# Kernel optimization log

Measured on AMD Instinct MI355X. Metric: run time of the kernel, lower is better.

## Reference

```python
import jax, jax.numpy as jnp
import numpy as np

N = 100000       # num_nodes
E = 1200000      # num_edges
D = 64           # input feature dim
K = 10           # propagation iterations
ALPHA = 0.1      # teleport probability
H0, H1 = 64, 32  # units_list


def setup_inputs() -> dict:
    key = jax.random.key(0)
    ks = jax.random.split(key, 5)
    x = jax.random.normal(ks[0], (N, D), dtype=jnp.float32)
    edge_index = jax.random.randint(ks[1], (2, E), 0, N, dtype=jnp.int32)
    edge_weight = jax.random.uniform(ks[2], (E,), dtype=jnp.float32)
    # glorot-ish dense params per units_list=[64, 32]
    W0 = jax.random.normal(ks[3], (D, H0), dtype=jnp.float32) * (1.0 / np.sqrt(D))
    b0 = jnp.zeros((H0,), jnp.float32)
    W1 = jax.random.normal(ks[4], (H0, H1), dtype=jnp.float32) * (1.0 / np.sqrt(H0))
    b1 = jnp.zeros((H1,), jnp.float32)
    return dict(x=x, edge_index=edge_index, edge_weight=edge_weight,
                W0=W0, b0=b0, W1=W1, b1=b1)


def reference(x, edge_index, edge_weight, W0, b0, W1, b1):
    n = x.shape[0]
    loop = jnp.arange(n, dtype=edge_index.dtype)
    # GCN renorm: add self-loops with fill weight 1, symmetric D^-1/2 A D^-1/2
    row = jnp.concatenate([edge_index[0], loop])
    col = jnp.concatenate([edge_index[1], loop])
    w = jnp.concatenate([edge_weight, jnp.ones((n,), x.dtype)])
    deg = jax.ops.segment_sum(w, row, num_segments=n)
    dinv = jax.lax.rsqrt(jnp.maximum(deg, 1e-12))
    nw = dinv[row] * w * dinv[col]          # [E+N] normalized edge weights

    # k-hop propagation with running sum: (1/K) sum_k A_hat^k x
    h = x
    acc = jnp.zeros_like(x)
    for _ in range(K):
        h = jax.ops.segment_sum(nw[:, None] * h[row], col, num_segments=n)
        acc = acc + h
    out = acc * ((1.0 - ALPHA) / K) + ALPHA * x

    # dense MLP stack: all but last activated with relu, last linear
    out = jax.nn.relu(out @ W0 + b0)
    out = out @ W1 + b1
    return out
```

## Files before the change

kernel.cpp:

```cpp
#include <hip/hip_runtime.h>
#include <hip/hip_bf16.h>

#define NTHREADS 256
#define GB 256
#define NB 256
#define BW 512

typedef unsigned int uint32;
typedef unsigned long long u64;
typedef __bf16 bf16x8 __attribute__((ext_vector_type(8)));
typedef float f32x4 __attribute__((ext_vector_type(4)));


__device__ __forceinline__ float blo(uint32 u) { return __uint_as_float(u << 16); }
__device__ __forceinline__ float bhi(uint32 u) { return __uint_as_float(u & 0xffff0000u); }

__device__ __forceinline__ unsigned short bf16bits(float f) {
    __hip_bfloat16 h = __float2bfloat16(f);
    return *reinterpret_cast<unsigned short*>(&h);
}
__device__ __forceinline__ uint32 pk2(float a, float b) {
    return (uint32)bf16bits(a) | ((uint32)bf16bits(b) << 16);
}


__global__ __launch_bounds__(256) void histcols_k(const int* __restrict__ row,
                                                  const int* __restrict__ col,
                                                  int* __restrict__ bh, int* __restrict__ bh2,
                                                  int e, int ch) {
    __shared__ int h1[NB], h2[NB];
    int tid = threadIdx.x;
    h1[tid] = 0; h2[tid] = 0;
    __syncthreads();
    int beg = blockIdx.x * ch;
    int end = min(e, beg + ch);
    for (int i = beg + tid; i < end; i += 256) {
        atomicAdd(&h1[col[i] >> 9], 1);
        atomicAdd(&h2[row[i] >> 9], 1);
    }
    __syncthreads();
    bh[(size_t)tid * GB + blockIdx.x] = h1[tid];
    bh2[(size_t)tid * GB + blockIdx.x] = h2[tid];
}


__global__ __launch_bounds__(256) void scanb_k(int* bh, int* tb) {
    __shared__ int s[GB];
    int b = blockIdx.x;
    int tid = threadIdx.x;
    size_t base = (size_t)b * GB + tid;
    int v = bh[base];
    s[tid] = v;
    __syncthreads();
    for (int off = 1; off < GB; off <<= 1) {
        int t = (tid >= off) ? s[tid - off] : 0;
        __syncthreads();
        s[tid] += t;
        __syncthreads();
    }
    bh[base] = s[tid] - v;
    if (tid == GB - 1) tb[b] = s[GB - 1];
}


__global__ void scant_k(const int* __restrict__ tb, int* gbase) {
    __shared__ int s[256];
    int tid = threadIdx.x;
    int v = tb[tid];
    s[tid] = v;
    __syncthreads();
    for (int off = 1; off < 256; off <<= 1) {
        int t = (tid >= off) ? s[tid - off] : 0;
        __syncthreads();
        s[tid] += t;
        __syncthreads();
    }
    gbase[tid] = s[tid] - v;
    if (tid == 255) gbase[256] = s[255];
}


__global__ __launch_bounds__(256) void bscatter_k(const int* __restrict__ row,
                                                  const int* __restrict__ col,
                                                  const float* __restrict__ w,
                                                  const int* __restrict__ bh,
                                                  const int* __restrict__ bh2,
                                                  const int* __restrict__ gb,
                                                  const int* __restrict__ gb2,
                                                  unsigned short* __restrict__ st_col,
                                                  u64* __restrict__ st_rw,
                                                  u64* __restrict__ st2,
                                                  int e, int ch) {
    __shared__ int h1[NB], h2[NB];
    int tid = threadIdx.x;
    h1[tid] = 0; h2[tid] = 0;
    __syncthreads();
    int beg = blockIdx.x * ch;
    int end = min(e, beg + ch);
    for (int i = beg + tid; i < end; i += 256) {
        int c = col[i], r = row[i];
        float wv = w[i];
        u64 rec = (u64)(uint32)r | ((u64)__float_as_uint(wv) << 32);
        int bk = c >> 9;
        int rank = atomicAdd(&h1[bk], 1);
        int slot = gb[bk] + bh[(size_t)bk * GB + blockIdx.x] + rank;
        st_col[slot] = (unsigned short)(c & (BW - 1));
        st_rw[slot] = rec;
        int bk2 = r >> 9;
        int rank2 = atomicAdd(&h2[bk2], 1);
        int slot2 = gb2[bk2] + bh2[(size_t)bk2 * GB + blockIdx.x] + rank2;
        st2[slot2] = rec;
    }
}


__global__ __launch_bounds__(256) void bdeg_k(const u64* __restrict__ st2,
                                              const int* __restrict__ gb2,
                                              float* __restrict__ dinv, int n) {
    __shared__ float facc[BW];
    int bk = blockIdx.x;
    int tid = threadIdx.x;
    facc[tid] = 0.f; facc[tid + 256] = 0.f;
    __syncthreads();
    int beg = gb2[bk], end = gb2[bk + 1];
    for (int j = beg + tid; j < end; j += 256) {
        u64 v = st2[j];
        int r = (int)(uint32)v;
        float wv = __uint_as_float((uint32)(v >> 32));
        atomicAdd(&facc[r & (BW - 1)], wv);
    }
    __syncthreads();
    int n0 = bk * BW + tid, n1 = n0 + 256;
    if (n0 < n) dinv[n0] = rsqrtf(fmaxf(facc[tid] + 1.f, 1e-12f));
    if (n1 < n) dinv[n1] = rsqrtf(fmaxf(facc[tid + 256] + 1.f, 1e-12f));
}


__global__ __launch_bounds__(256) void bcount_k(const unsigned short* __restrict__ st_col,
                                                const int* __restrict__ gb,
                                                int* __restrict__ counts, int n) {
    __shared__ int cnt[BW];
    int bk = blockIdx.x;
    int tid = threadIdx.x;
    cnt[tid] = 0; cnt[tid + 256] = 0;
    __syncthreads();
    int beg = gb[bk], end = gb[bk + 1];
    for (int j = beg + tid; j < end; j += 256)
        atomicAdd(&cnt[st_col[j]], 1);
    __syncthreads();
    int n0 = bk * BW + tid, n1 = n0 + 256;
    if (n0 < n) counts[n0] = cnt[tid];
    if (n1 < n) counts[n1] = cnt[tid + 256];
}


__global__ void scan1_k(const int* __restrict__ counts, int* offsets, int* blockSums, int n) {
    __shared__ int s[256];
    int tid = threadIdx.x;
    int idx = blockIdx.x * 256 + tid;
    int v = (idx < n) ? counts[idx] : 0;
    s[tid] = v;
    __syncthreads();
    for (int off = 1; off < 256; off <<= 1) {
        int t = (tid >= off) ? s[tid - off] : 0;
        __syncthreads();
        s[tid] += t;
        __syncthreads();
    }
    if (idx < n) offsets[idx] = s[tid] - v;
    if (tid == 255) blockSums[blockIdx.x] = s[255];
}

__global__ void scan2_k(int* blockSums, int nb) {
    __shared__ int s[1024];
    int tid = threadIdx.x;
    int v = (tid < nb) ? blockSums[tid] : 0;
    s[tid] = v;
    __syncthreads();
    for (int off = 1; off < 1024; off <<= 1) {
        int t = (tid >= off) ? s[tid - off] : 0;
        __syncthreads();
        s[tid] += t;
        __syncthreads();
    }
    if (tid < nb) blockSums[tid] = s[tid] - v;
}

__global__ void scan3_k(int* offsets, const int* __restrict__ blockSums, int n, int total) {
    int idx = blockIdx.x * blockDim.x + threadIdx.x;
    if (idx < n) offsets[idx] += blockSums[idx >> 8];
    if (idx == n) offsets[n] = total;
}


__global__ __launch_bounds__(256) void bplace_k(const unsigned short* __restrict__ st_col,
                                                const u64* __restrict__ st_rw,
                                                const int* __restrict__ gb,
                                                const int* __restrict__ offsets,
                                                u64* __restrict__ csr) {
    __shared__ int cnt[BW];
    int bk = blockIdx.x;
    int tid = threadIdx.x;
    cnt[tid] = 0; cnt[tid + 256] = 0;
    __syncthreads();
    int beg = gb[bk], end = gb[bk + 1];
    for (int j = beg + tid; j < end; j += 256) {
        int c9 = st_col[j];
        int rank = atomicAdd(&cnt[c9], 1);
        int node = (bk << 9) | c9;
        csr[offsets[node] + rank] = st_rw[j];
    }
}


__global__ void uxseed_k(const float* __restrict__ x, const float* __restrict__ dinv,
                         uint32* __restrict__ ux, int pairs) {
    int i = blockIdx.x * blockDim.x + threadIdx.x;
    if (i < pairs) {
        float di = dinv[i >> 5];
        float2 v = ((const float2*)x)[i];
        ux[i] = pk2(di * v.x, di * v.y);
    }
}


template <int MODE>
__global__ __launch_bounds__(256) void horner4n_k(
    const unsigned short* __restrict__ u_in,
    unsigned short* __restrict__ u_out,
    unsigned short* __restrict__ ybf,
    const unsigned short* __restrict__ ux_bf,
    const float* __restrict__ x,
    const float* __restrict__ dinv,
    const int* __restrict__ offsets,
    const u64* __restrict__ csr,
    int n)
{
    int wv = __builtin_amdgcn_readfirstlane(threadIdx.x >> 6);
    int lane = threadIdx.x & 63;
    int g = lane >> 3;
    int s = lane & 7;
    int nbase = blockIdx.x * 16 + wv * 4;

    int bb[4], ee[4];
#pragma unroll
    for (int m = 0; m < 4; ++m) {
        int node = nbase + m;
        if (node < n) { bb[m] = offsets[node]; ee[m] = offsets[node + 1]; }
        else          { bb[m] = 0; ee[m] = 0; }
    }
    int maxd = max(max(ee[0] - bb[0], ee[1] - bb[1]), max(ee[2] - bb[2], ee[3] - bb[3]));

    float acc[4][8];
#pragma unroll
    for (int m = 0; m < 4; ++m)
#pragma unroll
        for (int i = 0; i < 8; ++i) acc[m][i] = 0.f;

    u64 sw[4];
#pragma unroll
    for (int m = 0; m < 4; ++m) {
        int j = bb[m] + g;
        sw[m] = (j < ee[m]) ? csr[j] : 0ull;
    }

    for (int off = 0; off < maxd; off += 8) {
        uint4 q[4];
#pragma unroll
        for (int m = 0; m < 4; ++m)
            q[m] = ((const uint4*)(u_in + (size_t)(uint32)(sw[m] & 0xffffffffu) * 64))[s];
        u64 swn[4];
#pragma unroll
        for (int m = 0; m < 4; ++m) {
            int j = bb[m] + off + 8 + g;
            swn[m] = (j < ee[m]) ? csr[j] : 0ull;
        }
#pragma unroll
        for (int m = 0; m < 4; ++m) {
            float w = __uint_as_float((uint32)(sw[m] >> 32));
            acc[m][0] = fmaf(w, blo(q[m].x), acc[m][0]);
            acc[m][1] = fmaf(w, bhi(q[m].x), acc[m][1]);
            acc[m][2] = fmaf(w, blo(q[m].y), acc[m][2]);
            acc[m][3] = fmaf(w, bhi(q[m].y), acc[m][3]);
            acc[m][4] = fmaf(w, blo(q[m].z), acc[m][4]);
            acc[m][5] = fmaf(w, bhi(q[m].z), acc[m][5]);
            acc[m][6] = fmaf(w, blo(q[m].w), acc[m][6]);
            acc[m][7] = fmaf(w, bhi(q[m].w), acc[m][7]);
        }
#pragma unroll
        for (int m = 0; m < 4; ++m) sw[m] = swn[m];
    }

#pragma unroll
    for (int mask = 8; mask <= 32; mask <<= 1)
#pragma unroll
        for (int m = 0; m < 4; ++m)
#pragma unroll
            for (int i = 0; i < 8; ++i)
                acc[m][i] += __shfl_xor(acc[m][i], mask);

    float t[8];
#pragma unroll
    for (int i = 0; i < 8; ++i) {
        float a01 = (g == 0) ? acc[0][i] : acc[1][i];
        float a23 = (g == 2) ? acc[2][i] : acc[3][i];
        t[i] = (g < 2) ? a01 : a23;
    }

    if (g < 4) {
        int node = nbase + g;
        if (node < n) {
            float di = dinv[node];
            uint4 zq = ((const uint4*)(u_in + (size_t)node * 64))[s];
            t[0] += blo(zq.x); t[1] += bhi(zq.x);
            t[2] += blo(zq.y); t[3] += bhi(zq.y);
            t[4] += blo(zq.z); t[5] += bhi(zq.z);
            t[6] += blo(zq.w); t[7] += bhi(zq.w);
            if (MODE == 0) {
                float dd = di * di;
                uint4 xq = ((const uint4*)(ux_bf + (size_t)node * 64))[s];
                uint4 o;
                o.x = pk2(fmaf(dd, t[0], blo(xq.x)), fmaf(dd, t[1], bhi(xq.x)));
                o.y = pk2(fmaf(dd, t[2], blo(xq.y)), fmaf(dd, t[3], bhi(xq.y)));
                o.z = pk2(fmaf(dd, t[4], blo(xq.z)), fmaf(dd, t[5], bhi(xq.z)));
                o.w = pk2(fmaf(dd, t[6], blo(xq.w)), fmaf(dd, t[7], bhi(xq.w)));
                ((uint4*)(u_out + (size_t)node * 64))[s] = o;
            } else {
                float c = 0.09f * di;
                const float4* xr = (const float4*)(x + (size_t)node * 64);
                float4 xa = xr[s * 2], xb = xr[s * 2 + 1];
                uint4 o;
                o.x = pk2(fmaf(c, t[0], 0.1f * xa.x), fmaf(c, t[1], 0.1f * xa.y));
                o.y = pk2(fmaf(c, t[2], 0.1f * xa.z), fmaf(c, t[3], 0.1f * xa.w));
                o.z = pk2(fmaf(c, t[4], 0.1f * xb.x), fmaf(c, t[5], 0.1f * xb.y));
                o.w = pk2(fmaf(c, t[6], 0.1f * xb.z), fmaf(c, t[7], 0.1f * xb.w));
                ((uint4*)(ybf + (size_t)node * 64))[s] = o;
            }
        }
    }
}


__global__ __launch_bounds__(256) void mlp_mfma_k(const unsigned short* __restrict__ ybf,
                                                  const float* __restrict__ W0,
                                                  const float* __restrict__ b0,
                                                  const float* __restrict__ W1,
                                                  const float* __restrict__ b1,
                                                  float* __restrict__ out, int n) {
    __shared__ __align__(16) unsigned short W0t[64 * 64];
    __shared__ __align__(16) unsigned short W1t[32 * 64];
    __shared__ __align__(16) unsigned short hidL[4][16 * 64];
    __shared__ float b0s[64], b1s[32];
    int tid = threadIdx.x;
    for (int i = tid; i < 64 * 64; i += 256) {
        int k = i >> 6, j = i & 63;
        W0t[j * 64 + (k ^ ((j & 7) << 3))] = bf16bits(W0[i]);
    }
    for (int i = tid; i < 64 * 32; i += 256) {
        int k = i >> 5, j = i & 31;
        W1t[j * 64 + (k ^ ((j & 7) << 3))] = bf16bits(W1[i]);
    }
    if (tid < 64) b0s[tid] = b0[tid];
    else if (tid < 96) b1s[tid - 64] = b1[tid - 64];
    __syncthreads();

    int wave = tid >> 6, lane = tid & 63;
    int r = lane & 15, g = lane >> 4;
    int nbase = blockIdx.x * 64 + wave * 16;

    int nodeA = min(nbase + r, n - 1);
    const bf16x8* yrow = (const bf16x8*)(ybf + (size_t)nodeA * 64);
    bf16x8 A0 = yrow[g];
    bf16x8 A1 = yrow[4 + g];

#pragma unroll
    for (int t = 0; t < 4; ++t) {
        int j = t * 16 + r;
        int sj = j & 7;
        const bf16x8* wcol = (const bf16x8*)(W0t + j * 64);
        bf16x8 B0 = wcol[g ^ sj];
        bf16x8 B1 = wcol[(4 + g) ^ sj];
        float bv = b0s[j];
        f32x4 acc = {bv, bv, bv, bv};
        acc = __builtin_amdgcn_mfma_f32_16x16x32_bf16(A0, B0, acc, 0, 0, 0);
        acc = __builtin_amdgcn_mfma_f32_16x16x32_bf16(A1, B1, acc, 0, 0, 0);
#pragma unroll
        for (int v = 0; v < 4; ++v) {
            int i = g * 4 + v;
            hidL[wave][i * 64 + (j ^ ((i & 7) << 3))] = bf16bits(fmaxf(acc[v], 0.f));
        }
    }

    const bf16x8* hrow = (const bf16x8*)(hidL[wave] + r * 64);
    int sr = r & 7;
    bf16x8 HA0 = hrow[g ^ sr];
    bf16x8 HA1 = hrow[(4 + g) ^ sr];
#pragma unroll
    for (int t = 0; t < 2; ++t) {
        int j = t * 16 + r;
        int sj = j & 7;
        const bf16x8* wcol = (const bf16x8*)(W1t + j * 64);
        bf16x8 B0 = wcol[g ^ sj];
        bf16x8 B1 = wcol[(4 + g) ^ sj];
        float bv = b1s[j];
        f32x4 acc = {bv, bv, bv, bv};
        acc = __builtin_amdgcn_mfma_f32_16x16x32_bf16(HA0, B0, acc, 0, 0, 0);
        acc = __builtin_amdgcn_mfma_f32_16x16x32_bf16(HA1, B1, acc, 0, 0, 0);
#pragma unroll
        for (int v = 0; v < 4; ++v) {
            int node = nbase + g * 4 + v;
            if (node < n) out[(size_t)node * 32 + j] = acc[v];
        }
    }
}


extern "C" void kernel_launch(void* const* d_in, const int* in_sizes, int n_in,
                              void* d_out, int out_size, void* d_ws, size_t ws_size,
                              hipStream_t stream) {
    const float* x   = (const float*)d_in[0];
    const int*   ei  = (const int*)d_in[1];
    const float* ew  = (const float*)d_in[2];
    const float* W0  = (const float*)d_in[3];
    const float* b0  = (const float*)d_in[4];
    const float* W1  = (const float*)d_in[5];
    const float* b1  = (const float*)d_in[6];
    float* out = (float*)d_out;

    const int N = in_sizes[0] / 64;
    const int E = in_sizes[2];
    const int* row = ei;
    const int* col = ei + E;

    char* p = (char*)d_ws;
    auto alloc = [&](size_t bytes) -> void* {
        void* r = (void*)p;
        p += (bytes + 255) & ~(size_t)255;
        return r;
    };
    float* dinv      = (float*)alloc((size_t)N * 4);
    int*   bh        = (int*)alloc((size_t)NB * GB * 4);
    int*   bh2       = (int*)alloc((size_t)NB * GB * 4);
    int*   tb        = (int*)alloc(NB * 4);
    int*   tb2       = (int*)alloc(NB * 4);
    int*   gb        = (int*)alloc((NB + 1) * 4);
    int*   gb2       = (int*)alloc((NB + 1) * 4);
    unsigned short* st_col = (unsigned short*)alloc((size_t)E * 2);
    u64*   st_rw     = (u64*)alloc((size_t)E * 8);
    int*   counts    = (int*)alloc((size_t)N * 4);
    int*   offsets   = (int*)alloc((size_t)(N + 1) * 4);
    int    nb        = (N + 255) / 256;
    int*   blockSums = (int*)alloc((size_t)nb * 4);
    u64*   csr       = (u64*)alloc((size_t)E * 8);
    unsigned short* uxbf = (unsigned short*)alloc((size_t)N * 64 * 2);
    unsigned short* uA   = (unsigned short*)alloc((size_t)N * 64 * 2);
    unsigned short* uB   = (unsigned short*)alloc((size_t)N * 64 * 2);
    unsigned short* ybf  = (unsigned short*)alloc((size_t)N * 64 * 2);

    int ch = (E + GB - 1) / GB;

    histcols_k<<<GB, 256, 0, stream>>>(row, col, bh, bh2, E, ch);
    scanb_k<<<NB, 256, 0, stream>>>(bh, tb);
    scanb_k<<<NB, 256, 0, stream>>>(bh2, tb2);
    scant_k<<<1, 256, 0, stream>>>(tb, gb);
    scant_k<<<1, 256, 0, stream>>>(tb2, gb2);
    bscatter_k<<<GB, 256, 0, stream>>>(row, col, ew, bh, bh2, gb, gb2,
                                       st_col, st_rw, csr , E, ch);
    bdeg_k<<<NB, 256, 0, stream>>>(csr , gb2, dinv, N);
    bcount_k<<<NB, 256, 0, stream>>>(st_col, gb, counts, N);

    scan1_k<<<nb, 256, 0, stream>>>(counts, offsets, blockSums, N);
    scan2_k<<<1, 1024, 0, stream>>>(blockSums, nb);
    scan3_k<<<(N + 1 + NTHREADS - 1) / NTHREADS, NTHREADS, 0, stream>>>(offsets, blockSums, N, E);
    bplace_k<<<NB, 256, 0, stream>>>(st_col, st_rw, gb, offsets, csr);

    int pairs = N * 32;
    uxseed_k<<<(pairs + NTHREADS - 1) / NTHREADS, NTHREADS, 0, stream>>>(x, dinv,
                                                                         (uint32*)uxbf, pairs);

    int gP = (N + 15) / 16;
    const unsigned short* ui = uxbf;
    for (int k = 1; k <= 9; ++k) {
        unsigned short* uo = (ui == uA) ? uB : uA;
        horner4n_k<0><<<gP, 256, 0, stream>>>(ui, uo, nullptr, uxbf, x, dinv, offsets, csr, N);
        ui = uo;
    }
    horner4n_k<1><<<gP, 256, 0, stream>>>(ui, nullptr, ybf, uxbf, x, dinv, offsets, csr, N);

    mlp_mfma_k<<<(N + 63) / 64, 256, 0, stream>>>(ybf, W0, b0, W1, b1, out, N);
}
```

Baseline: 414.2 us.

## Stage bucket scatter through LDS for coalesced contiguous global writes

```diff
diff --git a/kernel.cpp b/kernel.cpp
--- a/kernel.cpp
+++ b/kernel.cpp
@@ -5,6 +5,7 @@
 #define GB 256
 #define NB 256
 #define BW 512
+#define CH 4864
 
 typedef unsigned int uint32;
 typedef unsigned long long u64;
@@ -80,36 +81,57 @@
 }
 
 
-__global__ __launch_bounds__(256) void bscatter_k(const int* __restrict__ row,
-                                                  const int* __restrict__ col,
-                                                  const float* __restrict__ w,
-                                                  const int* __restrict__ bh,
-                                                  const int* __restrict__ bh2,
-                                                  const int* __restrict__ gb,
-                                                  const int* __restrict__ gb2,
-                                                  unsigned short* __restrict__ st_col,
-                                                  u64* __restrict__ st_rw,
-                                                  u64* __restrict__ st2,
-                                                  int e, int ch) {
-    __shared__ int h1[NB], h2[NB];
-    int tid = threadIdx.x;
-    h1[tid] = 0; h2[tid] = 0;
-    __syncthreads();
-    int beg = blockIdx.x * ch;
-    int end = min(e, beg + ch);
+template <int WRITECOL>
+__global__ __launch_bounds__(256) void ldscat_k(const int* __restrict__ row,
+                                                const int* __restrict__ col,
+                                                const float* __restrict__ w,
+                                                const int* __restrict__ bh,
+                                                const int* __restrict__ gb,
+                                                unsigned short* __restrict__ st_col,
+                                                u64* __restrict__ st_rw,
+                                                int e, int ch) {
+    __shared__ u64 recs[CH];
+    __shared__ uint32 cidx[CH];
+    __shared__ int cnt[NB];
+    __shared__ int base[NB];
+    int tid = threadIdx.x, blk = blockIdx.x;
+    cnt[tid] = 0;
+    __syncthreads();
+    int beg = blk * ch, end = min(e, beg + ch);
+    const int* key = WRITECOL ? col : row;
+    for (int i = beg + tid; i < end; i += 256)
+        atomicAdd(&cnt[key[i] >> 9], 1);
+    __syncthreads();
+    int v = cnt[tid];
+    base[tid] = v;
+    __syncthreads();
+    for (int off = 1; off < 256; off <<= 1) {
+        int t = (tid >= off) ? base[tid - off] : 0;
+        __syncthreads();
+        base[tid] += t;
+        __syncthreads();
+    }
+    int excl = base[tid] - v;
+    __syncthreads();
+    base[tid] = excl;
+    cnt[tid] = excl;
+    __syncthreads();
     for (int i = beg + tid; i < end; i += 256) {
-        int c = col[i], r = row[i];
-        float wv = w[i];
-        u64 rec = (u64)(uint32)r | ((u64)__float_as_uint(wv) << 32);
-        int bk = c >> 9;
-        int rank = atomicAdd(&h1[bk], 1);
-        int slot = gb[bk] + bh[(size_t)bk * GB + blockIdx.x] + rank;
-        st_col[slot] = (unsigned short)(c & (BW - 1));
-        st_rw[slot] = rec;
-        int bk2 = r >> 9;
-        int rank2 = atomicAdd(&h2[bk2], 1);
-        int slot2 = gb2[bk2] + bh2[(size_t)bk2 * GB + blockIdx.x] + rank2;
-        st2[slot2] = rec;
+        int k = key[i];
+        int bk = k >> 9;
+        int p = atomicAdd(&cnt[bk], 1);
+        recs[p] = (u64)(uint32)row[i] | ((u64)__float_as_uint(w[i]) << 32);
+        cidx[p] = (uint32)((bk << 9) | (k & (BW - 1)));
+    }
+    __syncthreads();
+    int nblk = end - beg;
+    for (int j = tid; j < nblk; j += 256) {
+        uint32 ci = cidx[j];
+        int bk = ci >> 9;
+        int lrank = j - base[bk];
+        int slot = gb[bk] + bh[(size_t)bk * GB + blk] + lrank;
+        if (WRITECOL) st_col[slot] = (unsigned short)(ci & (BW - 1));
+        st_rw[slot] = recs[j];
     }
 }
 
@@ -464,8 +486,8 @@
     scanb_k<<<NB, 256, 0, stream>>>(bh2, tb2);
     scant_k<<<1, 256, 0, stream>>>(tb, gb);
     scant_k<<<1, 256, 0, stream>>>(tb2, gb2);
-    bscatter_k<<<GB, 256, 0, stream>>>(row, col, ew, bh, bh2, gb, gb2,
-                                       st_col, st_rw, csr , E, ch);
+    ldscat_k<1><<<GB, 256, 0, stream>>>(row, col, ew, bh, gb, st_col, st_rw, E, ch);
+    ldscat_k<0><<<GB, 256, 0, stream>>>(row, col, ew, bh2, gb2, nullptr, csr , E, ch);
     bdeg_k<<<NB, 256, 0, stream>>>(csr , gb2, dinv, N);
     bcount_k<<<NB, 256, 0, stream>>>(st_col, gb, counts, N);
 
```

After: 426.7 us. 1.03x slower.
